# Kernel optimization log

Hardware: AMD Instinct MI355X
Metric: run time of the kernel (lower is better)

The kernel has to match this reference:

```python
import jax, jax.numpy as jnp
import numpy as np


def setup_inputs() -> dict:
    key = jax.random.key(0)
    k1, k2 = jax.random.split(key)
    B, V, D = 2048, 2000, 64
    # multi-hot weights in [0,1); zeros denote absent categories
    inputs = jax.random.uniform(k1, (B, V), dtype=jnp.float32)
    # embedding table, uniform(-1, 1) as in Ludwig's default initializer
    embeddings = jax.random.uniform(k2, (V, D), dtype=jnp.float32, minval=-1.0, maxval=1.0)
    return {"inputs": inputs, "embeddings": embeddings}


def reference(inputs, embeddings):
    # inputs: (B, V) float weights; embeddings: (V, D)
    V = embeddings.shape[0]
    # signed_input = sign(abs(inputs)) -> 1 where nonzero, else 0
    # multiple_hot_indexes = signed_input * arange(V)  (zeros map to row 0)
    idx = jnp.where(inputs != 0, jnp.arange(V, dtype=jnp.int32)[None, :], 0)  # (B, V)
    gathered = embeddings[idx]  # (B, V, D) — dense lookup, as in the original
    # weighted multiply + sum-reduce over the vocab axis
    out = jnp.einsum("bv,bvd->bd", inputs, gathered)  # (B, D)
    return out
```

## Files before the change

kernel.cpp:

```cpp
#include <hip/hip_runtime.h>


#define Bn 2048
#define Vn 2000
#define Dn 64
#define KCH 16
#define KBLK 128
#define MBLK 64
#define LSTR 136

typedef __attribute__((ext_vector_type(8))) short bf16x8;
typedef __attribute__((ext_vector_type(4))) float f32x4;

__device__ inline unsigned short bf16r(float x) {
    union { float f; unsigned u; } c; c.f = x;
    return (unsigned short)((c.u + 0x8000u) >> 16);
}

__global__ __launch_bounds__(256)
void embw_mfma(const float* __restrict__ A, const float* __restrict__ E,
               float* __restrict__ part) {
    __shared__ unsigned short Al[MBLK][LSTR];
    __shared__ unsigned short Et[Dn][LSTR];

    const int t    = threadIdx.x;
    const int lane = t & 63;
    const int w    = t >> 6;
    const int kc   = blockIdx.x >> 5;
    const int mblk = blockIdx.x & 31;
    const int m0   = mblk * MBLK;
    const int k0   = kc * KBLK;

    {
        const int rs = t >> 5;
        const int c4 = t & 31;
        const int gk = k0 + c4 * 4;
        const bool real = (gk < Vn);
#pragma unroll
        for (int s = 0; s < 8; ++s) {
            const int row = s * 8 + rs;
            float4 v = make_float4(0.f, 0.f, 0.f, 0.f);
            if (real)
                v = *(const float4*)&A[(size_t)(m0 + row) * Vn + gk];
            unsigned lo = ((unsigned)bf16r(v.y) << 16) | bf16r(v.x);
            unsigned hi = ((unsigned)bf16r(v.w) << 16) | bf16r(v.z);
            *(uint2*)&Al[row][c4 * 4] = make_uint2(lo, hi);
        }
    }
    {
#pragma unroll
        for (int i = 0; i < KBLK / 4; ++i) {
            const int k  = w * (KBLK / 4) + i;
            const int gk = k0 + k;
            float v = (gk < Vn) ? E[(size_t)gk * Dn + lane] : 0.f;
            Et[lane][k] = bf16r(v);
        }
    }
    __syncthreads();

    const int fr = lane & 15;
    const int fk = (lane >> 4) * 8;
    f32x4 acc0 = {0.f, 0.f, 0.f, 0.f};
    f32x4 acc1 = {0.f, 0.f, 0.f, 0.f};
    f32x4 acc2 = {0.f, 0.f, 0.f, 0.f};
    f32x4 acc3 = {0.f, 0.f, 0.f, 0.f};
#pragma unroll
    for (int ks = 0; ks < KBLK / 32; ++ks) {
        const int kb = ks * 32 + fk;
        bf16x8 af = *(const bf16x8*)&Al[w * 16 + fr][kb];
        bf16x8 b0 = *(const bf16x8*)&Et[ 0 + fr][kb];
        bf16x8 b1 = *(const bf16x8*)&Et[16 + fr][kb];
        bf16x8 b2 = *(const bf16x8*)&Et[32 + fr][kb];
        bf16x8 b3 = *(const bf16x8*)&Et[48 + fr][kb];
        acc0 = __builtin_amdgcn_mfma_f32_16x16x32_bf16(af, b0, acc0, 0, 0, 0);
        acc1 = __builtin_amdgcn_mfma_f32_16x16x32_bf16(af, b1, acc1, 0, 0, 0);
        acc2 = __builtin_amdgcn_mfma_f32_16x16x32_bf16(af, b2, acc2, 0, 0, 0);
        acc3 = __builtin_amdgcn_mfma_f32_16x16x32_bf16(af, b3, acc3, 0, 0, 0);
    }

    float* pp = part + ((size_t)kc * Bn + m0 + w * 16 + (lane >> 4) * 4) * Dn + fr;
#pragma unroll
    for (int q = 0; q < 4; ++q) {
        pp[(size_t)q * Dn +  0] = acc0[q];
        pp[(size_t)q * Dn + 16] = acc1[q];
        pp[(size_t)q * Dn + 32] = acc2[q];
        pp[(size_t)q * Dn + 48] = acc3[q];
    }
}

__global__ __launch_bounds__(256)
void embw_reduce(const float* __restrict__ part, float* __restrict__ out) {
    const int i = blockIdx.x * 256 + threadIdx.x;
    const float4* p = (const float4*)part;
    float4 s = p[i];
#pragma unroll
    for (int c = 1; c < KCH; ++c) {
        float4 tv = p[(size_t)c * (Bn * Dn / 4) + i];
        s.x += tv.x; s.y += tv.y; s.z += tv.z; s.w += tv.w;
    }
    ((float4*)out)[i] = s;
}

extern "C" void kernel_launch(void* const* d_in, const int* in_sizes, int n_in,
                              void* d_out, int out_size, void* d_ws, size_t ws_size,
                              hipStream_t stream) {
    const float* in  = (const float*)d_in[0];
    const float* emb = (const float*)d_in[1];
    float* out  = (float*)d_out;
    float* part = (float*)d_ws;

    const int grid1 = 32 * KCH;
    embw_mfma<<<grid1, 256, 0, stream>>>(in, emb, part);

    const int grid2 = (Bn * Dn / 4) / 256;
    embw_reduce<<<grid2, 256, 0, stream>>>(part, out);
}
```

Before: 79.56 us.

## Pre-pack embedding table into MFMA B-fragment layout in a separate kernel

```diff
diff --git a/kernel.cpp b/kernel.cpp
--- a/kernel.cpp
+++ b/kernel.cpp
@@ -8,6 +8,8 @@
 #define KBLK 128
 #define MBLK 64
 #define LSTR 136
+#define NKS 64
+#define EFRAG_FLOATS 65536
 
 typedef __attribute__((ext_vector_type(8))) short bf16x8;
 typedef __attribute__((ext_vector_type(4))) float f32x4;
@@ -18,10 +20,30 @@
 }
 
 __global__ __launch_bounds__(256)
-void embw_mfma(const float* __restrict__ A, const float* __restrict__ E,
+void efrag_k(const float* __restrict__ E, uint4* __restrict__ ef) {
+    const int ks   = blockIdx.x;
+    const int ct   = threadIdx.x >> 6;
+    const int lane = threadIdx.x & 63;
+    const int d    = ct * 16 + (lane & 15);
+    const int kb   = ks * 32 + (lane >> 4) * 8;
+    unsigned short h[8];
+#pragma unroll
+    for (int j = 0; j < 8; ++j) {
+        const int gk = kb + j;
+        h[j] = (gk < Vn) ? bf16r(E[(size_t)gk * Dn + d]) : (unsigned short)0;
+    }
+    uint4 v;
+    v.x = (unsigned)h[0] | ((unsigned)h[1] << 16);
+    v.y = (unsigned)h[2] | ((unsigned)h[3] << 16);
+    v.z = (unsigned)h[4] | ((unsigned)h[5] << 16);
+    v.w = (unsigned)h[6] | ((unsigned)h[7] << 16);
+    ef[((size_t)ks * 4 + ct) * 64 + lane] = v;
+}
+
+__global__ __launch_bounds__(256)
+void embw_mfma(const float* __restrict__ A, const bf16x8* __restrict__ ef,
                float* __restrict__ part) {
     __shared__ unsigned short Al[MBLK][LSTR];
-    __shared__ unsigned short Et[Dn][LSTR];
 
     const int t    = threadIdx.x;
     const int lane = t & 63;
@@ -47,31 +69,22 @@
             *(uint2*)&Al[row][c4 * 4] = make_uint2(lo, hi);
         }
     }
-    {
-#pragma unroll
-        for (int i = 0; i < KBLK / 4; ++i) {
-            const int k  = w * (KBLK / 4) + i;
-            const int gk = k0 + k;
-            float v = (gk < Vn) ? E[(size_t)gk * Dn + lane] : 0.f;
-            Et[lane][k] = bf16r(v);
-        }
-    }
     __syncthreads();
 
     const int fr = lane & 15;
     const int fk = (lane >> 4) * 8;
-    f32x4 acc0 = {0.f, 0.f, 0.f, 0.f};
-    f32x4 acc1 = {0.f, 0.f, 0.f, 0.f};
-    f32x4 acc2 = {0.f, 0.f, 0.f, 0.f};
-    f32x4 acc3 = {0.f, 0.f, 0.f, 0.f};
+    f32x4 acc0 = {0.f,0.f,0.f,0.f}, acc1 = {0.f,0.f,0.f,0.f};
+    f32x4 acc2 = {0.f,0.f,0.f,0.f}, acc3 = {0.f,0.f,0.f,0.f};
+
 #pragma unroll
     for (int ks = 0; ks < KBLK / 32; ++ks) {
-        const int kb = ks * 32 + fk;
-        bf16x8 af = *(const bf16x8*)&Al[w * 16 + fr][kb];
-        bf16x8 b0 = *(const bf16x8*)&Et[ 0 + fr][kb];
-        bf16x8 b1 = *(const bf16x8*)&Et[16 + fr][kb];
-        bf16x8 b2 = *(const bf16x8*)&Et[32 + fr][kb];
-        bf16x8 b3 = *(const bf16x8*)&Et[48 + fr][kb];
+        const int ksg = kc * 4 + ks;
+        const size_t eb = ((size_t)ksg * 4) * 64 + lane;
+        bf16x8 af = *(const bf16x8*)&Al[w * 16 + fr][ks * 32 + fk];
+        bf16x8 b0 = ef[eb +   0];
+        bf16x8 b1 = ef[eb +  64];
+        bf16x8 b2 = ef[eb + 128];
+        bf16x8 b3 = ef[eb + 192];
         acc0 = __builtin_amdgcn_mfma_f32_16x16x32_bf16(af, b0, acc0, 0, 0, 0);
         acc1 = __builtin_amdgcn_mfma_f32_16x16x32_bf16(af, b1, acc1, 0, 0, 0);
         acc2 = __builtin_amdgcn_mfma_f32_16x16x32_bf16(af, b2, acc2, 0, 0, 0);
@@ -106,12 +119,12 @@
                               hipStream_t stream) {
     const float* in  = (const float*)d_in[0];
     const float* emb = (const float*)d_in[1];
-    float* out  = (float*)d_out;
-    float* part = (float*)d_ws;
+    float* out = (float*)d_out;
 
-    const int grid1 = 32 * KCH;
-    embw_mfma<<<grid1, 256, 0, stream>>>(in, emb, part);
+    uint4* efrag = (uint4*)d_ws;
+    float* part  = (float*)d_ws + EFRAG_FLOATS;
 
-    const int grid2 = (Bn * Dn / 4) / 256;
-    embw_reduce<<<grid2, 256, 0, stream>>>(part, out);
+    efrag_k<<<NKS, 256, 0, stream>>>(emb, efrag);
+    embw_mfma<<<32 * KCH, 256, 0, stream>>>(in, (const bf16x8*)efrag, part);
+    embw_reduce<<<(Bn * Dn / 4) / 256, 256, 0, stream>>>(part, out);
 }
```

After: 74.28 us. 1.07x faster.
